# Performance work log

Measured on AMD Instinct MI355X. Metric: run time of the kernel, lower is better.

Reference implementation:

```python
import jax, jax.numpy as jnp
import numpy as np

E = 768       # embed dim
NH = 12       # heads
HD = 64       # head dim
WIN = 14      # window size
DEPTH = 12
PATCH = 16
WINDOW_IDX = (0, 1, 3, 4, 6, 7, 9, 10)
EPS = 1e-6


def layer_norm(x, w, b):
    mu = jnp.mean(x, axis=-1, keepdims=True)
    var = jnp.mean(jnp.square(x - mu), axis=-1, keepdims=True)
    return (x - mu) * jax.lax.rsqrt(var + EPS) * w + b


def get_rel_pos(size, rel_pos):
    # q_size == k_size -> direct lookup, no interpolation
    coords = jnp.arange(size)
    rel = coords[:, None] - coords[None, :] + (size - 1)
    return rel_pos[rel]  # (size, size, HD)


def attention(x, qkv_w, qkv_b, proj_w, proj_b, rel_h, rel_w):
    B, H, W, _ = x.shape
    N = H * W
    qkv = (x.reshape(B, N, E) @ qkv_w + qkv_b).reshape(B, N, 3, NH, HD)
    q = qkv[:, :, 0].transpose(0, 2, 1, 3).reshape(B * NH, N, HD)
    k = qkv[:, :, 1].transpose(0, 2, 1, 3).reshape(B * NH, N, HD)
    v = qkv[:, :, 2].transpose(0, 2, 1, 3).reshape(B * NH, N, HD)
    attn = (q * (HD ** -0.5)) @ k.transpose(0, 2, 1)  # (B*NH, N, N)
    # decomposed relative position bias
    Rh = get_rel_pos(H, rel_h)  # (H, H, HD)
    Rw = get_rel_pos(W, rel_w)  # (W, W, HD)
    r_q = q.reshape(B * NH, H, W, HD)
    rh = jnp.einsum('bhwc,hkc->bhwk', r_q, Rh)
    rw = jnp.einsum('bhwc,wkc->bhwk', r_q, Rw)
    attn = attn.reshape(B * NH, H, W, H, W) + rh[:, :, :, :, None] + rw[:, :, :, None, :]
    attn = jax.nn.softmax(attn.reshape(B * NH, N, N), axis=-1)
    out = (attn @ v).reshape(B, NH, H, W, HD).transpose(0, 2, 3, 1, 4).reshape(B, H, W, E)
    return out @ proj_w + proj_b


def window_partition(x, ws):
    B, H, W, C = x.shape
    pad_h, pad_w = (-H) % ws, (-W) % ws
    x = jnp.pad(x, ((0, 0), (0, pad_h), (0, pad_w), (0, 0)))
    Hp, Wp = H + pad_h, W + pad_w
    x = x.reshape(B, Hp // ws, ws, Wp // ws, ws, C).transpose(0, 1, 3, 2, 4, 5)
    return x.reshape(-1, ws, ws, C), (Hp, Wp)


def window_unpartition(win, ws, pad_hw, hw):
    Hp, Wp = pad_hw
    H, W = hw
    B = win.shape[0] // ((Hp // ws) * (Wp // ws))
    x = win.reshape(B, Hp // ws, Wp // ws, ws, ws, -1).transpose(0, 1, 3, 2, 4, 5)
    return x.reshape(B, Hp, Wp, -1)[:, :H, :W]


def _forward(x, patch_w, patch_b, pos_embed,
             ln1_w, ln1_b, qkv_w, qkv_b, proj_w, proj_b,
             rel_h_win, rel_w_win, rel_h_glob, rel_w_glob,
             ln2_w, ln2_b, fc1_w, fc1_b, fc2_w, fc2_b, out_w, out_b):
    # patch embed: conv 16x16 stride 16
    x = jax.lax.conv_general_dilated(
        x, patch_w, (PATCH, PATCH), 'VALID',
        dimension_numbers=('NCHW', 'OIHW', 'NCHW'))
    x = x.transpose(0, 2, 3, 1) + patch_b  # (B, H, W, C)
    x = x + pos_embed
    win_i, glob_i = 0, 0
    for i in range(DEPTH):
        shortcut = x
        h = layer_norm(x, ln1_w[i], ln1_b[i])
        if i in WINDOW_IDX:
            hw = h.shape[1:3]
            h, pad_hw = window_partition(h, WIN)
            h = attention(h, qkv_w[i], qkv_b[i], proj_w[i], proj_b[i],
                          rel_h_win[win_i], rel_w_win[win_i])
            h = window_unpartition(h, WIN, pad_hw, hw)
            win_i += 1
        else:
            h = attention(h, qkv_w[i], qkv_b[i], proj_w[i], proj_b[i],
                          rel_h_glob[glob_i], rel_w_glob[glob_i])
            glob_i += 1
        x = shortcut + h
        h = layer_norm(x, ln2_w[i], ln2_b[i])
        h = jax.nn.gelu(h @ fc1_w[i] + fc1_b[i], approximate=False) @ fc2_w[i] + fc2_b[i]
        x = x + h
    feat = x.transpose(0, 3, 1, 2)  # (B, C, H, W) == 'last_feat'
    return jnp.einsum('bchw,oc->bohw', feat, out_w) + out_b[None, :, None, None]


def setup_inputs() -> dict:
    key = jax.random.key(0)
    ks = iter(jax.random.split(key, 64))
    def n(shape, s=0.02):
        return jax.random.normal(next(ks), shape, jnp.float32) * s
    B, IMG = 2, 512
    G = IMG // PATCH  # 32
    return {
        'x': jax.random.normal(next(ks), (B, 3, IMG, IMG), jnp.float32),
        'patch_w': n((E, 3, PATCH, PATCH)),
        'patch_b': jnp.zeros((E,), jnp.float32),
        'pos_embed': n((1, G, G, E)),
        'ln1_w': jnp.ones((DEPTH, E), jnp.float32),
        'ln1_b': jnp.zeros((DEPTH, E), jnp.float32),
        'qkv_w': n((DEPTH, E, 3 * E)),
        'qkv_b': jnp.zeros((DEPTH, 3 * E), jnp.float32),
        'proj_w': n((DEPTH, E, E)),
        'proj_b': jnp.zeros((DEPTH, E), jnp.float32),
        'rel_h_win': n((8, 2 * WIN - 1, HD)),
        'rel_w_win': n((8, 2 * WIN - 1, HD)),
        'rel_h_glob': n((4, 2 * G - 1, HD)),
        'rel_w_glob': n((4, 2 * G - 1, HD)),
        'ln2_w': jnp.ones((DEPTH, E), jnp.float32),
        'ln2_b': jnp.zeros((DEPTH, E), jnp.float32),
        'fc1_w': n((DEPTH, E, 4 * E)),
        'fc1_b': jnp.zeros((DEPTH, 4 * E), jnp.float32),
        'fc2_w': n((DEPTH, 4 * E, E)),
        'fc2_b': jnp.zeros((DEPTH, E), jnp.float32),
        'out_w': n((256, E)),
        'out_b': jnp.zeros((256,), jnp.float32),
    }


def reference(x, patch_w, patch_b, pos_embed,
              ln1_w, ln1_b, qkv_w, qkv_b, proj_w, proj_b,
              rel_h_win, rel_w_win, rel_h_glob, rel_w_glob,
              ln2_w, ln2_b, fc1_w, fc1_b, fc2_w, fc2_b, out_w, out_b):
    return _forward(x, patch_w, patch_b, pos_embed,
                    ln1_w, ln1_b, qkv_w, qkv_b, proj_w, proj_b,
                    rel_h_win, rel_w_win, rel_h_glob, rel_w_glob,
                    ln2_w, ln2_b, fc1_w, fc1_b, fc2_w, fc2_b, out_w, out_b)
```

## Files before the change

kernel.cpp:

```cpp
#include <hip/hip_runtime.h>
#include <hip/hip_bf16.h>
#include <math.h>

static constexpr int E   = 768;
static constexpr int NH  = 12;
static constexpr int HD  = 64;
static constexpr int Bsz = 2;
static constexpr int G   = 32;
static constexpr int NTOK = G * G;
static constexpr int ROWS = Bsz * NTOK;
static constexpr int WS  = 14;
static constexpr int NWIN_SIDE = 3;
static constexpr int NWIN = NWIN_SIDE * NWIN_SIDE;
static constexpr int BW  = Bsz * NWIN;
static constexpr int NW  = WS * WS;
static constexpr int WROWS = BW * NW;
static constexpr int WIN_MASK = 0x6DB;

typedef __attribute__((ext_vector_type(8))) short short8;
typedef __attribute__((ext_vector_type(4))) float f32x4;
typedef unsigned short ushort_t;

__device__ __forceinline__ unsigned short f2bf(float x) {
  union { float f; unsigned u; } v; v.f = x;
  unsigned r = v.u + 0x7fffu + ((v.u >> 16) & 1u);
  return (unsigned short)(r >> 16);
}
__device__ __forceinline__ float bf2f(unsigned short h) {
  union { unsigned u; float f; } v; v.u = ((unsigned)h) << 16;
  return v.f;
}

__device__ __forceinline__ void glds16(const void* g, void* l) {
  __builtin_amdgcn_global_load_lds(
      (const __attribute__((address_space(1))) unsigned*)g,
      (__attribute__((address_space(3))) unsigned*)l, 16, 0, 0);
}

__global__ __launch_bounds__(256) void ln_kernel(
    const float* __restrict__ in, const float* __restrict__ w,
    const float* __restrict__ b, ushort_t* __restrict__ out) {
  const int wave = threadIdx.x >> 6, lane = threadIdx.x & 63;
  const int row = blockIdx.x * 4 + wave;
  const float4* r4 = (const float4*)(in + (size_t)row * E);
  float4 v[3];
  v[0] = r4[lane]; v[1] = r4[lane + 64]; v[2] = r4[lane + 128];
  float s = 0.f, s2 = 0.f;
#pragma unroll
  for (int i = 0; i < 3; i++) {
    s += v[i].x + v[i].y + v[i].z + v[i].w;
    s2 += v[i].x * v[i].x + v[i].y * v[i].y + v[i].z * v[i].z + v[i].w * v[i].w;
  }
#pragma unroll
  for (int off = 1; off <= 32; off <<= 1) {
    s += __shfl_xor(s, off);
    s2 += __shfl_xor(s2, off);
  }
  const float mean = s * (1.f / E);
  const float var  = s2 * (1.f / E) - mean * mean;
  const float rs   = rsqrtf(var + 1e-6f);
  ushort_t* o = out + (size_t)row * E;
#pragma unroll
  for (int i = 0; i < 3; i++) {
    const int e0 = (lane + i * 64) * 4;
    ushort4 p;
    p.x = f2bf((v[i].x - mean) * rs * w[e0]     + b[e0]);
    p.y = f2bf((v[i].y - mean) * rs * w[e0 + 1] + b[e0 + 1]);
    p.z = f2bf((v[i].z - mean) * rs * w[e0 + 2] + b[e0 + 2]);
    p.w = f2bf((v[i].w - mean) * rs * w[e0 + 3] + b[e0 + 3]);
    *(ushort4*)&o[e0] = p;
  }
}

enum { OP_QKV = 0, OP_GELU = 1, OP_ADD = 2, OP_POS = 3, OP_HEAD = 4 };

template <int OP, int MAP>
__global__ __launch_bounds__(256) void gemm_bt(
    const ushort_t* __restrict__ A, const ushort_t* __restrict__ Bt,
    const float* __restrict__ bias, const float* __restrict__ res,
    const float* __restrict__ pos, void* __restrict__ Cp,
    int M, int N, int K, int ncol) {
  __shared__ ushort_t As[2][64 * 64];
  __shared__ ushort_t Bs[2][64 * 64];
  const int tid = threadIdx.x, wave = tid >> 6, lane = tid & 63;
  const int lx = lane & 15, ly = lane >> 4;

  const int nwg = gridDim.x;
  const int q = nwg >> 3, r = nwg & 7;
  const int xcd = blockIdx.x & 7, loc = blockIdx.x >> 3;
  const int wgid = ((xcd < r) ? xcd * (q + 1) : r * (q + 1) + (xcd - r) * q) + loc;
  const int brow = wgid / ncol, bcol = wgid - brow * ncol;
  const int row0 = brow * 64, col0 = bcol * 64;
  const int wm = (wave >> 1) * 32, wn = (wave & 1) * 32;
  const int rin = lane >> 3, pseg = lane & 7;
  const int lseg = pseg ^ rin;
  f32x4 acc[2][2] = {};

  const ushort_t* aptr[2];
  const ushort_t* bptr[2];
#pragma unroll
  for (int j = 0; j < 2; j++) {
    const int slot = wave * 2 + j;
    int ar = row0 + slot * 8 + rin;
    if (ar >= M) ar = M - 1;
    if (MAP == 2) {
      const int bI = ar >> 10, t = ar & 1023, y = t >> 5, x = t & 31;
      const int by = y / WS, wy = y - by * WS;
      const int bx = x / WS, wx = x - bx * WS;
      const int win = bI * NWIN + by * NWIN_SIDE + bx;
      aptr[j] = &A[((size_t)win * NW + wy * WS + wx) * E + lseg * 8];
    } else {
      aptr[j] = &A[(size_t)ar * K + lseg * 8];
    }
    const int br = col0 + slot * 8 + rin;
    bptr[j] = &Bt[(size_t)br * K + lseg * 8];
  }

#pragma unroll
  for (int j = 0; j < 2; j++) {
    const int slot = wave * 2 + j;
    glds16(aptr[j], &As[0][slot * 512]);
    glds16(bptr[j], &Bs[0][slot * 512]);
  }

  const int nt = K >> 6;
  for (int t = 0; t < nt; t++) {
    const int cur = t & 1;
    if (t + 1 < nt) {
      const int k1 = (t + 1) << 6;
#pragma unroll
      for (int j = 0; j < 2; j++) {
        const int slot = wave * 2 + j;
        glds16(aptr[j] + k1, &As[cur ^ 1][slot * 512]);
        glds16(bptr[j] + k1, &Bs[cur ^ 1][slot * 512]);
      }
      asm volatile("s_waitcnt vmcnt(4)" ::: "memory");
    } else {
      asm volatile("s_waitcnt vmcnt(0)" ::: "memory");
    }
    __builtin_amdgcn_s_barrier();
    __builtin_amdgcn_sched_barrier(0);
#pragma unroll
    for (int kb = 0; kb < 2; kb++) {
      short8 af[2], bfm[2];
#pragma unroll
      for (int m = 0; m < 2; m++) {
        const int rr = wm + m * 16 + lx;
        af[m] = *(const short8*)&As[cur][rr * 64 + (((kb * 4 + ly) ^ (rr & 7)) * 8)];
      }
#pragma unroll
      for (int n = 0; n < 2; n++) {
        const int rr = wn + n * 16 + lx;
        bfm[n] = *(const short8*)&Bs[cur][rr * 64 + (((kb * 4 + ly) ^ (rr & 7)) * 8)];
      }
      __builtin_amdgcn_s_setprio(1);
#pragma unroll
      for (int m = 0; m < 2; m++)
#pragma unroll
        for (int n = 0; n < 2; n++)
          acc[m][n] = __builtin_amdgcn_mfma_f32_16x16x32_bf16(af[m], bfm[n], acc[m][n], 0, 0, 0);
      __builtin_amdgcn_s_setprio(0);
    }
    asm volatile("s_waitcnt lgkmcnt(0)" ::: "memory");
    __builtin_amdgcn_s_barrier();
    __builtin_amdgcn_sched_barrier(0);
  }

#pragma unroll
  for (int m = 0; m < 2; m++) {
#pragma unroll
    for (int r4 = 0; r4 < 4; r4++) {
      const int gr = row0 + wm + m * 16 + ly * 4 + r4;
      if (gr >= M) continue;
#pragma unroll
      for (int n = 0; n < 2; n++) {
        const int gc = col0 + wn + n * 16 + lx;
        float v = acc[m][n][r4] + bias[gc];
        if (OP == OP_GELU) v = 0.5f * v * (1.f + erff(v * 0.70710678118654752f));
        if (OP == OP_ADD)  v += res[(size_t)gr * N + gc];
        if (OP == OP_POS)  v += pos[(size_t)(gr & 1023) * N + gc];
        if (OP == OP_QKV || OP == OP_GELU)
          ((ushort_t*)Cp)[(size_t)gr * N + gc] = f2bf(v);
        else if (OP == OP_HEAD)
          ((float*)Cp)[(((size_t)(gr >> 10) * 256 + gc) << 10) | (gr & 1023)] = v;
        else
          ((float*)Cp)[(size_t)gr * N + gc] = v;
      }
    }
  }
}

__global__ __launch_bounds__(128) void attn_mfma(
    const ushort_t* __restrict__ qkv, ushort_t* __restrict__ out,
    const float* __restrict__ relh, const float* __restrict__ relw,
    int Hd, int Wd) {
  const int Ntok = Hd * Wd;
  __shared__ ushort_t smem[11392];
  ushort_t* Ks   = smem;
  ushort_t* Vst  = smem + 2048;
  ushort_t* Ps   = smem + 4608;
  ushort_t* Qs   = smem;
  ushort_t* RelS = smem + 2048;
  ushort_t* Th   = smem + 6144;
  ushort_t* Tw   = smem + 8256;
  ushort_t* khw  = smem + 10368;

  const int tid = threadIdx.x, wave = tid >> 6, lane = tid & 63;
  const int lx = lane & 15, ly = lane >> 4;
  const int bh = blockIdx.y, b = bh / NH, nh = bh % NH;
  const int q0 = blockIdx.x * 32;
  const size_t base = (size_t)b * Ntok * 2304 + nh * 64;

#pragma unroll
  for (int i = 0; i < 2; i++) {
    const int fv = i * 128 + tid;
    const int row = fv >> 3, dv8 = (fv & 7) * 8;
    const int qq = min(q0 + row, Ntok - 1);
    short8 v = *(const short8*)&qkv[base + (size_t)qq * 2304 + dv8];
    *(short8*)&Qs[(row * 64 + dv8) ^ ((row & 7) << 3)] = v;
  }
  for (int k = tid; k < 1024; k += 128) {
    const int kc = min(k, Ntok - 1);
    const int kh = kc / Wd;
    khw[k] = (ushort_t)((kh << 8) | (kc - kh * Wd));
  }
  __syncthreads();

  short8 qa[2];
  {
    const int row = wave * 16 + lx;
#pragma unroll
    for (int kb = 0; kb < 2; kb++)
      qa[kb] = *(const short8*)&Qs[(row * 64 + kb * 32 + ly * 8) ^ ((row & 7) << 3)];
  }
  int qh_r[4], qw_r[4];
#pragma unroll
  for (int r = 0; r < 4; r++) {
    const int qc = min(q0 + wave * 16 + ly * 4 + r, Ntok - 1);
    qh_r[r] = qc / Wd;
    qw_r[r] = qc - qh_r[r] * Wd;
  }

  for (int t = 0; t < 2; t++) {
    const float* rel = t ? relw : relh;
    const int TR = t ? (2 * Wd - 1) : (2 * Hd - 1);
    __syncthreads();
#pragma unroll
    for (int i = 0; i < 4; i++) {
      const int fv = i * 128 + tid;
      const int row = fv >> 3, c8 = (fv & 7) * 8;
      short8 v = {};
      if (row < TR) {
        const float* rp = &rel[(size_t)row * 64 + c8];
        const float4 a = *(const float4*)rp;
        const float4 bq = *(const float4*)(rp + 4);
        v[0] = (short)f2bf(a.x);  v[1] = (short)f2bf(a.y);
        v[2] = (short)f2bf(a.z);  v[3] = (short)f2bf(a.w);
        v[4] = (short)f2bf(bq.x); v[5] = (short)f2bf(bq.y);
        v[6] = (short)f2bf(bq.z); v[7] = (short)f2bf(bq.w);
      }
      *(short8*)&RelS[(row * 64 + c8) ^ ((row & 7) << 3)] = v;
    }
    __syncthreads();
    const int NT = (TR + 15) >> 4;
    ushort_t* T = t ? Tw : Th;
    for (int nt = 0; nt < NT; nt++) {
      f32x4 a = {};
      __builtin_amdgcn_s_setprio(1);
#pragma unroll
      for (int kb = 0; kb < 2; kb++) {
        const int rrow = nt * 16 + lx;
        short8 bfv = *(const short8*)&RelS[(rrow * 64 + kb * 32 + ly * 8) ^ ((rrow & 7) << 3)];
        a = __builtin_amdgcn_mfma_f32_16x16x32_bf16(qa[kb], bfv, a, 0, 0, 0);
      }
      __builtin_amdgcn_s_setprio(0);
#pragma unroll
      for (int reg = 0; reg < 4; reg++)
        T[(wave * 16 + ly * 4 + reg) * 66 + nt * 16 + lx] = f2bf(a[reg]);
    }
  }

  f32x4 o[4] = {};
  float m_[4], l_[4];
#pragma unroll
  for (int r = 0; r < 4; r++) { m_[r] = -3e38f; l_[r] = 0.f; }

  const int nkt = (Ntok + 31) >> 5;
  const int srow = tid >> 3, c7 = tid & 7, dv8s = c7 * 8;
  const int vswz = (c7 & 3) << 3;

  short8 kpre[2], vpre[2];
#pragma unroll
  for (int i = 0; i < 2; i++) {
    const int gk = srow + i * 16;
    short8 kv = {}, vv = {};
    if (gk < Ntok) {
      kv = *(const short8*)&qkv[base + 768 + (size_t)gk * 2304 + dv8s];
      vv = *(const short8*)&qkv[base + 1536 + (size_t)gk * 2304 + dv8s];
    }
    kpre[i] = kv; vpre[i] = vv;
  }

  for (int kt = 0; kt < nkt; kt++) {
    __syncthreads();
#pragma unroll
    for (int i = 0; i < 2; i++) {
      const int row = srow + i * 16;
      *(short8*)&Ks[(row * 64 + dv8s) ^ ((row & 7) << 3)] = kpre[i];
      const int kcol = row ^ vswz;
#pragma unroll
      for (int j = 0; j < 8; j++)
        Vst[(dv8s + j) * 40 + kcol] = (ushort_t)vpre[i][j];
    }
    if (kt + 1 < nkt) {
#pragma unroll
      for (int i = 0; i < 2; i++) {
        const int gk = (kt + 1) * 32 + srow + i * 16;
        short8 kv = {}, vv = {};
        if (gk < Ntok) {
          kv = *(const short8*)&qkv[base + 768 + (size_t)gk * 2304 + dv8s];
          vv = *(const short8*)&qkv[base + 1536 + (size_t)gk * 2304 + dv8s];
        }
        kpre[i] = kv; vpre[i] = vv;
      }
    }
    __syncthreads();

    f32x4 c[2] = {};
    __builtin_amdgcn_s_setprio(1);
#pragma unroll
    for (int kb = 0; kb < 2; kb++)
#pragma unroll
      for (int ct = 0; ct < 2; ct++) {
        const int krow = ct * 16 + lx;
        short8 kf = *(const short8*)&Ks[(krow * 64 + kb * 32 + ly * 8) ^ ((krow & 7) << 3)];
        c[ct] = __builtin_amdgcn_mfma_f32_16x16x32_bf16(qa[kb], kf, c[ct], 0, 0, 0);
      }
    __builtin_amdgcn_s_setprio(0);

    const int k0a = kt * 32 + lx, k1a = k0a + 16;
    const int tv0 = khw[k0a], tv1 = khw[k1a];
    const int kh0 = tv0 >> 8, kw0 = tv0 & 255;
    const int kh1 = tv1 >> 8, kw1 = tv1 & 255;
    float pv0[4], pv1[4], mt[4];
#pragma unroll
    for (int r = 0; r < 4; r++) {
      const int trow = (wave * 16 + ly * 4 + r) * 66;
      float s0 = c[0][r] * 0.125f + bf2f(Th[trow + qh_r[r] - kh0 + Hd - 1])
               + bf2f(Tw[trow + qw_r[r] - kw0 + Wd - 1]);
      float s1 = c[1][r] * 0.125f + bf2f(Th[trow + qh_r[r] - kh1 + Hd - 1])
               + bf2f(Tw[trow + qw_r[r] - kw1 + Wd - 1]);
      if (k0a >= Ntok) s0 = -1e30f;
      if (k1a >= Ntok) s1 = -1e30f;
      pv0[r] = s0; pv1[r] = s1;
      mt[r] = fmaxf(s0, s1);
    }
    const float dmax = fmaxf(fmaxf(mt[0] - m_[0], mt[1] - m_[1]),
                             fmaxf(mt[2] - m_[2], mt[3] - m_[3]));
    if (!__all(dmax <= 8.f)) {
#pragma unroll
      for (int r = 0; r < 4; r++) {
        float mr = mt[r];
#pragma unroll
        for (int off = 1; off <= 8; off <<= 1) mr = fmaxf(mr, __shfl_xor(mr, off));
        const float mn = fmaxf(m_[r], mr);
        const float sc = __expf(m_[r] - mn);
        m_[r] = mn; l_[r] *= sc;
#pragma unroll
        for (int dt = 0; dt < 4; dt++) o[dt][r] *= sc;
      }
    }
#pragma unroll
    for (int r = 0; r < 4; r++) {
      const float p0 = __expf(pv0[r] - m_[r]);
      const float p1 = __expf(pv1[r] - m_[r]);
      l_[r] += p0 + p1;
      const int pb = wave * 640 + (ly * 4 + r) * 40;
      Ps[pb + lx]      = f2bf(p0);
      Ps[pb + 16 + lx] = f2bf(p1);
    }
    short8 pf = *(const short8*)&Ps[wave * 640 + lx * 40 + ly * 8];
    __builtin_amdgcn_s_setprio(1);
#pragma unroll
    for (int dt = 0; dt < 4; dt++) {
      const int drow = dt * 16 + lx;
      short8 vf = *(const short8*)&Vst[drow * 40 + ((ly * 8) ^ (((drow >> 3) & 3) << 3))];
      o[dt] = __builtin_amdgcn_mfma_f32_16x16x32_bf16(pf, vf, o[dt], 0, 0, 0);
    }
    __builtin_amdgcn_s_setprio(0);
  }

#pragma unroll
  for (int r = 0; r < 4; r++) {
#pragma unroll
    for (int off = 1; off <= 8; off <<= 1) l_[r] += __shfl_xor(l_[r], off);
    const int qq = q0 + wave * 16 + ly * 4 + r;
    if (qq >= Ntok) continue;
    const float inv = 1.f / l_[r];
#pragma unroll
    for (int dt = 0; dt < 4; dt++)
      out[((size_t)b * Ntok + qq) * E + nh * 64 + dt * 16 + lx] = f2bf(o[dt][r] * inv);
  }
}

__global__ __launch_bounds__(128) void qkv_winpart(
    const ushort_t* __restrict__ qi, const float* __restrict__ qkvb,
    ushort_t* __restrict__ qw) {
  const int row = blockIdx.x;
  const int win = row / NW, t = row - win * NW;
  const int wy = t / WS, wx = t - wy * WS;
  const int b = win / NWIN, wr = win - b * NWIN;
  const int by = wr / NWIN_SIDE, bx = wr - by * NWIN_SIDE;
  const int y = by * WS + wy, x = bx * WS + wx;
  short8* dst = (short8*)(qw + (size_t)row * 2304);
  if (y < G && x < G) {
    const short8* src = (const short8*)(qi + (((size_t)b * G + y) * G + x) * 2304);
    for (int e = threadIdx.x; e < 288; e += 128) dst[e] = src[e];
  } else {
    for (int e = threadIdx.x; e < 288; e += 128) {
      short8 v;
#pragma unroll
      for (int j = 0; j < 8; j++) v[j] = (short)f2bf(qkvb[e * 8 + j]);
      dst[e] = v;
    }
  }
}

__global__ __launch_bounds__(256) void im2col(const float* __restrict__ x,
                                              ushort_t* __restrict__ out) {
  const int blk = blockIdx.x;
  const int b = blk >> 10, t = blk & 1023, gy = t >> 5, gx = t & 31;
  for (int k = threadIdx.x; k < 768; k += 256) {
    const int ci = k >> 8, rem = k & 255, py = rem >> 4, px = rem & 15;
    out[(size_t)blk * 768 + k] =
        f2bf(x[(((size_t)b * 3 + ci) * 512 + gy * 16 + py) * 512 + gx * 16 + px]);
  }
}

__global__ __launch_bounds__(256) void prep_wt64(
    const float* __restrict__ qkvw, const float* __restrict__ projw,
    const float* __restrict__ fc1w, const float* __restrict__ fc2w,
    ushort_t* __restrict__ wq, ushort_t* __restrict__ wp,
    ushort_t* __restrict__ w1, ushort_t* __restrict__ w2) {
  __shared__ float tile[64][65];
  const int blk = blockIdx.x;
  const float* W; ushort_t* Wt; int Kd, Nd, tn, tk;
  if (blk < 432)       { W = qkvw;  Wt = wq; Kd = 768;  Nd = 2304; tn = blk % 36;          tk = blk / 36; }
  else if (blk < 576)  { W = projw; Wt = wp; Kd = 768;  Nd = 768;  tn = (blk - 432) % 12;  tk = (blk - 432) / 12; }
  else if (blk < 1152) { W = fc1w;  Wt = w1; Kd = 768;  Nd = 3072; tn = (blk - 576) % 48;  tk = (blk - 576) / 48; }
  else                 { W = fc2w;  Wt = w2; Kd = 3072; Nd = 768;  tn = (blk - 1152) % 12; tk = (blk - 1152) / 12; }
  const int k0 = tk * 64, n0 = tn * 64;
  const int kr = threadIdx.x >> 2, cg = (threadIdx.x & 3) * 16;
  const float* src = &W[(size_t)(k0 + kr) * Nd + n0 + cg];
#pragma unroll
  for (int j = 0; j < 4; j++) {
    const float4 v = *(const float4*)&src[j * 4];
    tile[kr][cg + j * 4 + 0] = v.x;
    tile[kr][cg + j * 4 + 1] = v.y;
    tile[kr][cg + j * 4 + 2] = v.z;
    tile[kr][cg + j * 4 + 3] = v.w;
  }
  __syncthreads();
  const int nr = kr;
  short8 o0, o1;
#pragma unroll
  for (int j = 0; j < 8; j++) o0[j] = (short)f2bf(tile[cg + j][nr]);
#pragma unroll
  for (int j = 0; j < 8; j++) o1[j] = (short)f2bf(tile[cg + 8 + j][nr]);
  ushort_t* dst = &Wt[(size_t)(n0 + nr) * Kd + k0 + cg];
  *(short8*)&dst[0] = o0;
  *(short8*)&dst[8] = o1;
}

__global__ __launch_bounds__(256) void cast_bf16(const float* __restrict__ in,
                                                 ushort_t* __restrict__ out, int n) {
  const int idx = (blockIdx.x * 256 + threadIdx.x) * 4;
  if (idx + 3 < n) {
    const float4 v = *(const float4*)&in[idx];
    ushort4 p;
    p.x = f2bf(v.x); p.y = f2bf(v.y); p.z = f2bf(v.z); p.w = f2bf(v.w);
    *(ushort4*)&out[idx] = p;
  }
}

extern "C" void kernel_launch(void* const* d_in, const int* in_sizes, int n_in,
                              void* d_out, int out_size, void* d_ws, size_t ws_size,
                              hipStream_t stream) {
  const float* x_in     = (const float*)d_in[0];
  const float* patch_w  = (const float*)d_in[1];
  const float* patch_b  = (const float*)d_in[2];
  const float* pos_emb  = (const float*)d_in[3];
  const float* ln1_w    = (const float*)d_in[4];
  const float* ln1_b    = (const float*)d_in[5];
  const float* qkv_w    = (const float*)d_in[6];
  const float* qkv_b    = (const float*)d_in[7];
  const float* proj_w   = (const float*)d_in[8];
  const float* proj_b   = (const float*)d_in[9];
  const float* rel_h_w  = (const float*)d_in[10];
  const float* rel_w_w  = (const float*)d_in[11];
  const float* rel_h_g  = (const float*)d_in[12];
  const float* rel_w_g  = (const float*)d_in[13];
  const float* ln2_w    = (const float*)d_in[14];
  const float* ln2_b    = (const float*)d_in[15];
  const float* fc1_w    = (const float*)d_in[16];
  const float* fc1_b    = (const float*)d_in[17];
  const float* fc2_w    = (const float*)d_in[18];
  const float* fc2_b    = (const float*)d_in[19];
  const float* out_w    = (const float*)d_in[20];
  const float* out_b    = (const float*)d_in[21];
  float* outp = (float*)d_out;

  float* xbuf = (float*)d_ws;
  ushort_t* hb16    = (ushort_t*)(xbuf + (size_t)ROWS * E);
  ushort_t* qkvimg  = hb16 + (size_t)ROWS * E;
  ushort_t* qkvwin  = qkvimg + (size_t)ROWS * 3 * E;
  ushort_t* attnw16 = qkvwin + (size_t)WROWS * 3 * E;
  ushort_t* h1b16   = attnw16 + (size_t)WROWS * E;
  ushort_t* wq      = h1b16 + (size_t)ROWS * 4 * E;
  ushort_t* wp      = wq + (size_t)2304 * 768;
  ushort_t* w1      = wp + (size_t)768 * 768;
  ushort_t* w2      = w1 + (size_t)3072 * 768;
  ushort_t* pwT16   = w2 + (size_t)768 * 3072;
  ushort_t* headW16 = pwT16 + (size_t)768 * 768;
  ushort_t* imb16 = hb16;

  cast_bf16<<<576, 256, 0, stream>>>(patch_w, pwT16, 768 * 768);
  cast_bf16<<<192, 256, 0, stream>>>(out_w, headW16, 256 * 768);

  im2col<<<ROWS, 256, 0, stream>>>(x_in, imb16);
  gemm_bt<OP_POS, 0><<<12 * 32, 256, 0, stream>>>(
      imb16, pwT16, patch_b, nullptr, pos_emb, xbuf, ROWS, E, E, 12);

  int win_i = 0, glob_i = 0;
  for (int i = 0; i < 12; i++) {
    const bool is_win = (WIN_MASK >> i) & 1;

    prep_wt64<<<1728, 256, 0, stream>>>(
        qkv_w + (size_t)i * E * 3 * E, proj_w + (size_t)i * E * E,
        fc1_w + (size_t)i * E * 4 * E, fc2_w + (size_t)i * 4 * E * E,
        wq, wp, w1, w2);

    ln_kernel<<<ROWS / 4, 256, 0, stream>>>(xbuf, ln1_w + i * E, ln1_b + i * E, hb16);

    gemm_bt<OP_QKV, 0><<<36 * 32, 256, 0, stream>>>(
        hb16, wq, qkv_b + i * 3 * E, nullptr, nullptr, qkvimg, ROWS, 3 * E, E, 36);

    if (is_win) {
      qkv_winpart<<<WROWS, 128, 0, stream>>>(qkvimg, qkv_b + i * 3 * E, qkvwin);
      attn_mfma<<<dim3(7, BW * NH), 128, 0, stream>>>(
          qkvwin, attnw16, rel_h_w + (size_t)win_i * (2 * WS - 1) * HD,
          rel_w_w + (size_t)win_i * (2 * WS - 1) * HD, WS, WS);
      win_i++;
      gemm_bt<OP_ADD, 2><<<12 * 32, 256, 0, stream>>>(
          attnw16, wp, proj_b + i * E, xbuf, nullptr, xbuf, ROWS, E, E, 12);
    } else {
      attn_mfma<<<dim3(32, Bsz * NH), 128, 0, stream>>>(
          qkvimg, attnw16, rel_h_g + (size_t)glob_i * (2 * G - 1) * HD,
          rel_w_g + (size_t)glob_i * (2 * G - 1) * HD, G, G);
      glob_i++;
      gemm_bt<OP_ADD, 0><<<12 * 32, 256, 0, stream>>>(
          attnw16, wp, proj_b + i * E, xbuf, nullptr, xbuf, ROWS, E, E, 12);
    }

    ln_kernel<<<ROWS / 4, 256, 0, stream>>>(xbuf, ln2_w + i * E, ln2_b + i * E, hb16);
    gemm_bt<OP_GELU, 0><<<48 * 32, 256, 0, stream>>>(
        hb16, w1, fc1_b + i * 4 * E, nullptr, nullptr, h1b16, ROWS, 4 * E, E, 48);
    gemm_bt<OP_ADD, 0><<<12 * 32, 256, 0, stream>>>(
        h1b16, w2, fc2_b + i * E, xbuf, nullptr, xbuf, ROWS, E, 4 * E, 12);
  }

  cast_bf16<<<1536, 256, 0, stream>>>(xbuf, hb16, ROWS * E);
  gemm_bt<OP_HEAD, 0><<<4 * 32, 256, 0, stream>>>(
      hb16, headW16, out_b, nullptr, nullptr, outp, ROWS, 256, E, 4);
}
```

Baseline: 1.826 ms.

## Use 128x128 tiled GEMM kernel for QKV and FC1 projections

Adds a gemm_128 kernel in which each workgroup computes a 128x128 output tile, with each of its four waves owning a 64x64 sub-tile and 16 MFMA accumulators. The QKV and FC1 GEMMs switch to it, which cuts the workgroup count and raises operand reuse per LDS load. The new kernel stages through a single LDS buffer instead of double buffering, so global-to-LDS loads no longer overlap compute. The higher register use and the smaller grid (288 and 384 workgroups) may also lower occupancy on a 256-CU device.

```diff
diff --git a/kernel.cpp b/kernel.cpp
--- a/kernel.cpp
+++ b/kernel.cpp
@@ -73,6 +73,93 @@
 }
 
 enum { OP_QKV = 0, OP_GELU = 1, OP_ADD = 2, OP_POS = 3, OP_HEAD = 4 };
+
+template <int OP>
+__global__ __launch_bounds__(256) void gemm_128(
+    const ushort_t* __restrict__ A, const ushort_t* __restrict__ Bt,
+    const float* __restrict__ bias, const float* __restrict__ res,
+    const float* __restrict__ pos, void* __restrict__ Cp,
+    int M, int N, int K, int ncol) {
+  __shared__ ushort_t As[128 * 64];
+  __shared__ ushort_t Bs[128 * 64];
+  const int tid = threadIdx.x, wave = tid >> 6, lane = tid & 63;
+  const int lx = lane & 15, ly = lane >> 4;
+
+  const int nwg = gridDim.x;
+  const int q = nwg >> 3, r = nwg & 7;
+  const int xcd = blockIdx.x & 7, loc = blockIdx.x >> 3;
+  const int wgid = ((xcd < r) ? xcd * (q + 1) : r * (q + 1) + (xcd - r) * q) + loc;
+  const int brow = wgid / ncol, bcol = wgid - brow * ncol;
+  const int row0 = brow * 128, col0 = bcol * 128;
+  const int wm = (wave >> 1) * 64, wn = (wave & 1) * 64;
+  const int rin = lane >> 3, pseg = lane & 7;
+  const int lseg = pseg ^ rin;
+  f32x4 acc[4][4] = {};
+
+  const ushort_t* aptr[4];
+  const ushort_t* bptr[4];
+#pragma unroll
+  for (int j = 0; j < 4; j++) {
+    const int instr = wave * 4 + j;
+    int ar = row0 + instr * 8 + rin;
+    if (ar >= M) ar = M - 1;
+    aptr[j] = &A[(size_t)ar * K + lseg * 8];
+    const int br = col0 + instr * 8 + rin;
+    bptr[j] = &Bt[(size_t)br * K + lseg * 8];
+  }
+
+  for (int k0 = 0; k0 < K; k0 += 64) {
+    __syncthreads();
+#pragma unroll
+    for (int j = 0; j < 4; j++) {
+      const int instr = wave * 4 + j;
+      glds16(aptr[j] + k0, &As[instr * 512]);
+      glds16(bptr[j] + k0, &Bs[instr * 512]);
+    }
+    __syncthreads();
+#pragma unroll
+    for (int kb = 0; kb < 2; kb++) {
+      short8 af[4], bfm[4];
+#pragma unroll
+      for (int m = 0; m < 4; m++) {
+        const int rr = wm + m * 16 + lx;
+        af[m] = *(const short8*)&As[rr * 64 + (((kb * 4 + ly) ^ (rr & 7)) * 8)];
+      }
+#pragma unroll
+      for (int n = 0; n < 4; n++) {
+        const int rr = wn + n * 16 + lx;
+        bfm[n] = *(const short8*)&Bs[rr * 64 + (((kb * 4 + ly) ^ (rr & 7)) * 8)];
+      }
+      __builtin_amdgcn_s_setprio(1);
+#pragma unroll
+      for (int m = 0; m < 4; m++)
+#pragma unroll
+        for (int n = 0; n < 4; n++)
+          acc[m][n] = __builtin_amdgcn_mfma_f32_16x16x32_bf16(af[m], bfm[n], acc[m][n], 0, 0, 0);
+      __builtin_amdgcn_s_setprio(0);
+    }
+  }
+
+#pragma unroll
+  for (int m = 0; m < 4; m++) {
+#pragma unroll
+    for (int r4 = 0; r4 < 4; r4++) {
+      const int gr = row0 + wm + m * 16 + ly * 4 + r4;
+      if (gr >= M) continue;
+#pragma unroll
+      for (int n = 0; n < 4; n++) {
+        const int gc = col0 + wn + n * 16 + lx;
+        float v = acc[m][n][r4] + bias[gc];
+        if (OP == OP_GELU) v = 0.5f * v * (1.f + erff(v * 0.70710678118654752f));
+        if (OP == OP_ADD)  v += res[(size_t)gr * N + gc];
+        if (OP == OP_QKV || OP == OP_GELU)
+          ((ushort_t*)Cp)[(size_t)gr * N + gc] = f2bf(v);
+        else
+          ((float*)Cp)[(size_t)gr * N + gc] = v;
+      }
+    }
+  }
+}
 
 template <int OP, int MAP>
 __global__ __launch_bounds__(256) void gemm_bt(
@@ -542,8 +629,8 @@
 
     ln_kernel<<<ROWS / 4, 256, 0, stream>>>(xbuf, ln1_w + i * E, ln1_b + i * E, hb16);
 
-    gemm_bt<OP_QKV, 0><<<36 * 32, 256, 0, stream>>>(
-        hb16, wq, qkv_b + i * 3 * E, nullptr, nullptr, qkvimg, ROWS, 3 * E, E, 36);
+    gemm_128<OP_QKV><<<288, 256, 0, stream>>>(
+        hb16, wq, qkv_b + i * 3 * E, nullptr, nullptr, qkvimg, ROWS, 3 * E, E, 18);
 
     if (is_win) {
       qkv_winpart<<<WROWS, 128, 0, stream>>>(qkvimg, qkv_b + i * 3 * E, qkvwin);
@@ -563,8 +650,8 @@
     }
 
     ln_kernel<<<ROWS / 4, 256, 0, stream>>>(xbuf, ln2_w + i * E, ln2_b + i * E, hb16);
-    gemm_bt<OP_GELU, 0><<<48 * 32, 256, 0, stream>>>(
-        hb16, w1, fc1_b + i * 4 * E, nullptr, nullptr, h1b16, ROWS, 4 * E, E, 48);
+    gemm_128<OP_GELU><<<384, 256, 0, stream>>>(
+        hb16, w1, fc1_b + i * 4 * E, nullptr, nullptr, h1b16, ROWS, 4 * E, E, 24);
     gemm_bt<OP_ADD, 0><<<12 * 32, 256, 0, stream>>>(
         h1b16, w2, fc2_b + i * E, xbuf, nullptr, xbuf, ROWS, E, 4 * E, 12);
   }
```

After: 1.842 ms. About the same (+0.9%).
